# Optimization experiments

Hardware: AMD Instinct MI355X
Metric: run time of the kernel (lower is better)

Reference implementation:

```python
import jax, jax.numpy as jnp
import numpy as np

T, B = 32, 64
H, W = 16, 16
FEAT = 32
CNN_DIM = 512
N_ACT = 5
MAP_OUT = FEAT * H * W  # 8192, flattened map readout


def _conv_relu(x, w, b, stride):
    y = jax.lax.conv_general_dilated(
        x, w, (stride, stride), 'VALID',
        dimension_numbers=('NCHW', 'OIHW', 'NCHW'))
    return jax.nn.relu(y + b[None, :, None, None])


def _mlp(x, w1, b1, w2, b2):
    return jax.nn.relu(x @ w1 + b1) @ w2 + b2


def setup_inputs() -> dict:
    key = jax.random.key(0)
    ks = jax.random.split(key, 32)
    g = lambda k, shape, fan: jax.random.normal(k, shape, jnp.float32) * (1.0 / np.sqrt(fan))
    inp = {}
    inp['image'] = jax.random.uniform(ks[0], (T * B, 84, 84, 3), jnp.float32) * 255.0
    inp['done'] = jnp.zeros((T, B), jnp.float32)
    inp['state0'] = jnp.zeros((B, FEAT, H, W), jnp.float32)
    inp['position'] = jax.random.randint(ks[1], (T * B, 2), 0, H).astype(jnp.int32)
    # NatureCNN params
    inp['w1'] = g(ks[2], (32, 3, 8, 8), 3 * 8 * 8); inp['b1'] = jnp.zeros((32,), jnp.float32)
    inp['w2'] = g(ks[3], (64, 32, 4, 4), 32 * 4 * 4); inp['b2'] = jnp.zeros((64,), jnp.float32)
    inp['w3'] = g(ks[4], (64, 64, 3, 3), 64 * 3 * 3); inp['b3'] = jnp.zeros((64,), jnp.float32)
    inp['wfc'] = g(ks[5], (64 * 7 * 7, CNN_DIM), 64 * 7 * 7); inp['bfc'] = jnp.zeros((CNN_DIM,), jnp.float32)
    # Map write projection
    inp['Ww'] = g(ks[6], (CNN_DIM, FEAT), CNN_DIM); inp['bw'] = jnp.zeros((FEAT,), jnp.float32)
    # pos_net MLP: one-hot(16)+one-hot(16)=32 -> 64
    inp['wp1'] = g(ks[7], (2 * H, 64), 2 * H); inp['bp1'] = jnp.zeros((64,), jnp.float32)
    inp['wp2'] = g(ks[8], (64, 64), 64); inp['bp2'] = jnp.zeros((64,), jnp.float32)
    # policy MLP: (MAP_OUT+64) -> 64 -> N_ACT
    inp['wpo1'] = g(ks[9], (MAP_OUT + 64, 64), MAP_OUT + 64); inp['bpo1'] = jnp.zeros((64,), jnp.float32)
    inp['wpo2'] = g(ks[10], (64, N_ACT), 64) * 0.01; inp['bpo2'] = jnp.zeros((N_ACT,), jnp.float32)
    # value MLP
    inp['wv1'] = g(ks[11], (MAP_OUT + 64, 64), MAP_OUT + 64); inp['bv1'] = jnp.zeros((64,), jnp.float32)
    inp['wv2'] = g(ks[12], (64, 1), 64); inp['bv2'] = jnp.zeros((1,), jnp.float32)
    return inp


def reference(image, done, state0, w1, b1, w2, b2, w3, b3, wfc, bfc, Ww, bw,
              wp1, bp1, wp2, bp2, wpo1, bpo1, wpo2, bpo2, wv1, bv1, wv2, bv2,
              position):
    # preprocess_image: /255 and NHWC -> NCHW
    x = jnp.transpose(image / 255.0, (0, 3, 1, 2))
    x = _conv_relu(x, w1, b1, 4)   # [TB,32,20,20]
    x = _conv_relu(x, w2, b2, 2)   # [TB,64,9,9]
    x = _conv_relu(x, w3, b3, 1)   # [TB,64,7,7]
    h = jax.nn.relu(x.reshape(x.shape[0], -1) @ wfc + bfc)  # [TB,512]

    h_seq = h.reshape(T, B, CNN_DIM)
    idx_seq = position.reshape(T, B, 2)
    benv = jnp.arange(B)

    def step(state, inp):
        h_t, d_t, i_t = inp
        masked = (1.0 - d_t)[:, None, None, None] * state  # reset done envs
        wfeat = h_t @ Ww + bw                              # [B,FEAT]
        state = masked.at[benv, :, i_t[:, 0], i_t[:, 1]].add(wfeat)
        return state, state.reshape(B, -1)                 # per-step map readout

    state, outs = jax.lax.scan(step, state0, (h_seq, done, idx_seq))
    hidden = outs.reshape(T * B, MAP_OUT)

    # position net on one-hot coords
    pos_oh = jnp.concatenate([jax.nn.one_hot(position[:, 0], H, dtype=hidden.dtype),
                              jax.nn.one_hot(position[:, 1], W, dtype=hidden.dtype)], axis=1)
    pos_feat = _mlp(pos_oh, wp1, bp1, wp2, bp2)            # [TB,64]
    hidden = jnp.concatenate([hidden, pos_feat], axis=1)

    logits = _mlp(hidden, wpo1, bpo1, wpo2, bpo2)          # [TB,N_ACT]
    v = _mlp(hidden, wv1, bv1, wv2, bv2)                   # [TB,1]
    return logits, v, state
```

## Files before the change

kernel.cpp:

```cpp
#include <hip/hip_runtime.h>
#include <hip/hip_bf16.h>


#define TT 32
#define BB 64
#define TBR 2048

typedef _Float16 half_t;
typedef __attribute__((ext_vector_type(4))) _Float16 half4;
typedef __attribute__((ext_vector_type(8))) _Float16 half8;
typedef __attribute__((ext_vector_type(4))) float f32x4;

#define OFF_W1T   0u
#define OFF_W2T   6144u
#define OFF_W3T   22528u
#define OFF_WF    40960u
#define OFF_PF    106496u
#define OFF_Y0    237568u
#define OFF_YS    245760u
#define OFF_H     507904u
#define OFF_DELTA 1556480u
#define OFF_WFCT  1818624u
#define OFF_C3    2621440u
#define OFF_C2    5832704u
#define OFF_C1    11141120u

__global__ __launch_bounds__(256) void prep_all(
    const float* __restrict__ w1, const float* __restrict__ w2,
    const float* __restrict__ w3, half_t* __restrict__ w1p,
    half_t* __restrict__ w2T, half_t* __restrict__ w3T,
    const float* __restrict__ wfc, half_t* __restrict__ wfcT) {
  __shared__ float t[32][33];
  int bx = blockIdx.x;
  if (bx < 304) {
    int g = bx * 256 + threadIdx.x;
    if (g < 8192) {
      int kk = g & 31, oc = (g >> 5) & 31, tap = g >> 10;
      half_t v = (half_t)0.f;
      if (kk < 24) {
        int kx = kk / 3, c = kk - 3 * kx;
        v = (half_t)(w1[oc * 192 + c * 64 + tap * 8 + kx] * (1.0f / 255.0f));
      }
      w1p[g] = v;
      return;
    }
    int g2 = g - 8192;
    if (g2 < 32768) {
      int c = g2 & 31, oc = (g2 >> 5) & 63, tap = g2 >> 11;
      w2T[g2] = (half_t)w2[oc * 512 + c * 16 + tap];
      return;
    }
    int g3 = g2 - 32768;
    if (g3 < 36864) {
      int c = g3 & 63, oc = (g3 >> 6) & 63, tap = g3 >> 12;
      w3T[g3] = (half_t)w3[oc * 576 + c * 9 + tap];
    }
    return;
  }
  int gb = bx - 304;
  int k0 = (gb % 98) * 32, n0 = (gb / 98) * 32;
  int tx = threadIdx.x & 31, ty = threadIdx.x >> 5;
#pragma unroll
  for (int i = 0; i < 4; ++i)
    t[ty + 8 * i][tx] = wfc[(size_t)(k0 + ty + 8 * i) * 512 + n0 + tx];
  __syncthreads();
#pragma unroll
  for (int i = 0; i < 4; ++i)
    wfcT[(size_t)(n0 + ty + 8 * i) * 3136 + k0 + tx] =
        (half_t)t[tx][ty + 8 * i];
}

#define C1_BANDF 5040
#define C1_BANDV 1260
__global__ __launch_bounds__(256) void conv1_mfma(
    const float* __restrict__ img, const half_t* __restrict__ w1p,
    const float* __restrict__ b1, half_t* __restrict__ out, int n0) {
  __shared__ __align__(16) half_t As[2][C1_BANDF];
  int tid = threadIdx.x;
  int li = blockIdx.x;
  int w = tid >> 6, l = tid & 63, lc = l & 15, q = l >> 4;
  const float* ib = img + (size_t)(n0 + li) * 21168;
  half_t* ob = out + (size_t)li * 400 * 32;

  half8 bfrag[8][2];
#pragma unroll
  for (int tap = 0; tap < 8; ++tap)
#pragma unroll
    for (int t = 0; t < 2; ++t)
      bfrag[tap][t] =
          *(const half8*)(w1p + (size_t)(tap * 32 + t * 16 + lc) * 32 + q * 8);
  float b1v[2] = {b1[lc], b1[16 + lc]};

  f32x4 fr[5];
#define C1_LOADB(b)                                                   \
  {                                                                   \
    const float* src = ib + 4032 * (b);                               \
    _Pragma("unroll") for (int i = 0; i < 5; ++i) {                   \
      int g = tid + 256 * i;                                          \
      if (g < C1_BANDV) fr[i] = *(const f32x4*)(src + 4 * g);         \
    }                                                                 \
  }
#define C1_WRITEB(buf)                                                \
  {                                                                   \
    _Pragma("unroll") for (int i = 0; i < 5; ++i) {                   \
      int g = tid + 256 * i;                                          \
      if (g < C1_BANDV) {                                             \
        half4 o;                                                      \
        _Pragma("unroll") for (int j = 0; j < 4; ++j)                 \
            o[j] = (half_t)fr[i][j];                                  \
        *(half4*)&As[buf][4 * g] = o;                                 \
      }                                                               \
    }                                                                 \
  }

  C1_LOADB(0);
  C1_WRITEB(0);
  for (int b = 0; b < 5; ++b) {
    if (b < 4) C1_LOADB(b + 1);
    __syncthreads();
    int buf = b & 1;
    for (int tile = w; tile < 5; tile += 4) {
      int lp = tile * 16 + lc;
      int oyl = lp / 20, ox = lp - oyl * 20;
      f32x4 acc[2];
      acc[0] = (f32x4){0.f, 0.f, 0.f, 0.f};
      acc[1] = (f32x4){0.f, 0.f, 0.f, 0.f};
#pragma unroll
      for (int ky = 0; ky < 8; ++ky) {
        half8 af;
        if (q < 3) {
          const half_t* p = &As[buf][(4 * oyl + ky) * 252 + 12 * ox + q * 8];
          *(half4*)&af = *(const half4*)p;
          *((half4*)&af + 1) = *((const half4*)(p + 4));
        } else {
#pragma unroll
          for (int j = 0; j < 8; ++j) af[j] = (half_t)0.f;
        }
        acc[0] = __builtin_amdgcn_mfma_f32_16x16x32_f16(af, bfrag[ky][0],
                                                        acc[0], 0, 0, 0);
        acc[1] = __builtin_amdgcn_mfma_f32_16x16x32_f16(af, bfrag[ky][1],
                                                        acc[1], 0, 0, 0);
      }
#pragma unroll
      for (int t = 0; t < 2; ++t) {
#pragma unroll
        for (int r = 0; r < 4; ++r) {
          int mr = b * 80 + tile * 16 + q * 4 + r;
          ob[(size_t)mr * 32 + t * 16 + lc] =
              (half_t)fmaxf(acc[t][r] + b1v[t], 0.f);
        }
      }
    }
    if (b < 4) C1_WRITEB((b + 1) & 1);
  }
}

__global__ __launch_bounds__(256) void conv2_mfma(
    const half_t* __restrict__ in, const half_t* __restrict__ w2T,
    const float* __restrict__ b2, half_t* __restrict__ out, int n0) {
  __shared__ __align__(16) half_t As[12800];
  int tid = threadIdx.x;
  int li = blockIdx.x;
  int w = tid >> 6, l = tid & 63, lc = l & 15, q = l >> 4;
  const half_t* inb = in + (size_t)li * 12800;

#pragma unroll
  for (int i = 0; i < 7; ++i) {
    int ci = tid + 256 * i;
    if (ci < 1600) {
      uint4 v = *(const uint4*)(inb + ci * 8);
      int ip = ci >> 2, sp = ip >> 1;
      int u = ((ip & 1) << 6) | ((ci & 3) << 4);
      int byte = sp * 128 + (u ^ ((sp & 7) << 4));
      *(uint4*)((char*)As + byte) = v;
    }
  }

  half8 bfrag[16][2];
#pragma unroll
  for (int tap = 0; tap < 16; ++tap)
#pragma unroll
    for (int j = 0; j < 2; ++j) {
      int nt = (w & 1) * 2 + j;
      bfrag[tap][j] =
          *(const half8*)(w2T + (size_t)(tap * 64 + nt * 16 + lc) * 32 + q * 8);
    }
  float b2v[2];
#pragma unroll
  for (int j = 0; j < 2; ++j) b2v[j] = b2[(w & 1) * 32 + j * 16 + lc];

  __syncthreads();

  half_t* ob = out + (size_t)(n0 + li) * 5184;
#pragma unroll
  for (int ti = 0; ti < 3; ++ti) {
    int tile = (w >> 1) + 2 * ti;
    int row16 = tile * 16 + lc;
    int orow = row16 < 81 ? row16 : 80;
    int oy = orow / 9, ox = orow - oy * 9;
    f32x4 acc[2];
    acc[0] = (f32x4){0.f, 0.f, 0.f, 0.f};
    acc[1] = (f32x4){0.f, 0.f, 0.f, 0.f};
#pragma unroll
    for (int tap = 0; tap < 16; ++tap) {
      int ky = tap >> 2, kx = tap & 3;
      int ip = (2 * oy + ky) * 20 + 2 * ox + kx;
      int sp = ip >> 1;
      int u = ((ip & 1) << 6) | (q << 4);
      int byte = sp * 128 + (u ^ ((sp & 7) << 4));
      half8 af = *(const half8*)((const char*)As + byte);
      acc[0] = __builtin_amdgcn_mfma_f32_16x16x32_f16(af, bfrag[tap][0],
                                                      acc[0], 0, 0, 0);
      acc[1] = __builtin_amdgcn_mfma_f32_16x16x32_f16(af, bfrag[tap][1],
                                                      acc[1], 0, 0, 0);
    }
#pragma unroll
    for (int j = 0; j < 2; ++j) {
#pragma unroll
      for (int r = 0; r < 4; ++r) {
        int mr = tile * 16 + q * 4 + r;
        if (mr < 81) {
          int col = (w & 1) * 32 + j * 16 + lc;
          ob[(size_t)mr * 64 + col] = (half_t)fmaxf(acc[j][r] + b2v[j], 0.f);
        }
      }
    }
  }
}

__global__ __launch_bounds__(256) void conv3_mfma(
    const half_t* __restrict__ in, const half_t* __restrict__ w3T,
    const float* __restrict__ b3, half_t* __restrict__ out) {
  __shared__ __align__(16) half_t As[5184];
  int tid = threadIdx.x;
  int li = blockIdx.x;
  int w = tid >> 6, l = tid & 63, lc = l & 15, q = l >> 4;
  const half_t* inb = in + (size_t)li * 5184;

#pragma unroll
  for (int i = 0; i < 3; ++i) {
    int ci = tid + 256 * i;
    if (ci < 648) {
      uint4 v = *(const uint4*)(inb + ci * 8);
      int ir = ci >> 3, cc = ci & 7;
      int byte = ir * 128 + (((cc << 4)) ^ ((ir & 7) << 4));
      *(uint4*)((char*)As + byte) = v;
    }
  }

  half8 bfrag[9][2];
#pragma unroll
  for (int tap = 0; tap < 9; ++tap)
#pragma unroll
    for (int ch = 0; ch < 2; ++ch)
      bfrag[tap][ch] = *(const half8*)(
          w3T + (size_t)(tap * 64 + w * 16 + lc) * 64 + ch * 32 + q * 8);
  float b3v = b3[w * 16 + lc];

  __syncthreads();

  half_t* ob = out + (size_t)li * 3136;
#pragma unroll
  for (int tile = 0; tile < 4; ++tile) {
    int row16 = tile * 16 + lc;
    int orow = row16 < 49 ? row16 : 48;
    int oy = orow / 7, ox = orow - oy * 7;
    f32x4 acc = (f32x4){0.f, 0.f, 0.f, 0.f};
#pragma unroll
    for (int tap = 0; tap < 9; ++tap) {
      int ky = tap / 3, kx = tap - ky * 3;
      int ir = (oy + ky) * 9 + ox + kx;
#pragma unroll
      for (int ch = 0; ch < 2; ++ch) {
        int byte = ir * 128 + (((ch << 6) | (q << 4)) ^ ((ir & 7) << 4));
        half8 af = *(const half8*)((const char*)As + byte);
        acc = __builtin_amdgcn_mfma_f32_16x16x32_f16(af, bfrag[tap][ch],
                                                     acc, 0, 0, 0);
      }
    }
#pragma unroll
    for (int r = 0; r < 4; ++r) {
      int pos = tile * 16 + q * 4 + r;
      if (pos < 49) {
        int col = w * 16 + lc;
        ob[(size_t)col * 49 + pos] = (half_t)fmaxf(acc[r] + b3v, 0.f);
      }
    }
  }
}

__global__ __launch_bounds__(256) void fc_mfma(
    const half_t* __restrict__ A, const half_t* __restrict__ Bt,
    const float* __restrict__ bias, float* __restrict__ C) {
  __shared__ __align__(16) half_t As[64 * 40];
  __shared__ __align__(16) half_t Bs[64 * 40];
  int tid = threadIdx.x;
  int m0 = blockIdx.y * 64, n0 = blockIdx.x * 64;
  int w = tid >> 6;
  int l = tid & 63;
  int lc = l & 15, q = l >> 4;
  int srow = tid >> 2, sseg = tid & 3;

  const half_t* aPtr = A + (size_t)(m0 + srow) * 3136 + sseg * 8;
  const half_t* bPtr = Bt + (size_t)(n0 + srow) * 3136 + sseg * 8;
  uint4 aReg = *(const uint4*)aPtr;
  uint4 bReg = *(const uint4*)bPtr;

  f32x4 acc[4];
#pragma unroll
  for (int t = 0; t < 4; ++t) acc[t] = (f32x4){0.f, 0.f, 0.f, 0.f};

  for (int k0 = 0; k0 < 3136; k0 += 32) {
    __syncthreads();
    *(uint4*)&As[srow * 40 + sseg * 8] = aReg;
    *(uint4*)&Bs[srow * 40 + sseg * 8] = bReg;
    __syncthreads();
    if (k0 + 32 < 3136) {
      aReg = *(const uint4*)(aPtr + k0 + 32);
      bReg = *(const uint4*)(bPtr + k0 + 32);
    }
    half8 af = *(const half8*)&As[(w * 16 + lc) * 40 + q * 8];
#pragma unroll
    for (int t = 0; t < 4; ++t) {
      half8 bf = *(const half8*)&Bs[(t * 16 + lc) * 40 + q * 8];
      acc[t] = __builtin_amdgcn_mfma_f32_16x16x32_f16(af, bf, acc[t], 0, 0, 0);
    }
  }
#pragma unroll
  for (int t = 0; t < 4; ++t) {
#pragma unroll
    for (int r = 0; r < 4; ++r) {
      int row = m0 + w * 16 + q * 4 + r;
      int col = n0 + t * 16 + lc;
      C[(size_t)row * 512 + col] = fmaxf(acc[t][r] + bias[col], 0.f);
    }
  }
}

__global__ __launch_bounds__(256) void mid1_kernel(
    const float* __restrict__ h, const float* __restrict__ Ww,
    const float* __restrict__ bw, float* __restrict__ wf,
    const int* __restrict__ pos, const float* __restrict__ wp1,
    const float* __restrict__ bp1, const float* __restrict__ wp2,
    const float* __restrict__ bp2, float* __restrict__ pf,
    const float* __restrict__ s0, const float* __restrict__ wpo1,
    const float* __restrict__ wv1, float* __restrict__ y0) {
  __shared__ float red[128];
  int bx = blockIdx.x;
  if (bx < 256) {
    int g = bx * 256 + threadIdx.x;
    int row = g >> 5, oc = g & 31;
    float acc = bw[oc];
    const float* hr = h + (size_t)row * 512;
#pragma unroll 8
    for (int k = 0; k < 512; ++k) acc += hr[k] * Ww[k * 32 + oc];
    wf[g] = acc;
    return;
  }
  if (bx < 768) {
    int row = ((bx - 256) * 256 + threadIdx.x) >> 6;
    int l = threadIdx.x & 63;
    int p0 = pos[row * 2], p1 = pos[row * 2 + 1];
    float t1 = fmaxf(wp1[p0 * 64 + l] + wp1[(16 + p1) * 64 + l] + bp1[l], 0.f);
    float acc = bp2[l];
#pragma unroll
    for (int k = 0; k < 64; ++k) acc += __shfl(t1, k) * wp2[k * 64 + l];
    pf[row * 64 + l] = acc;
    return;
  }
  int g = bx - 768;
  int b = g >> 5, kc = g & 31;
  int n = threadIdx.x & 127, kh = threadIdx.x >> 7;
  const float* W = (n < 64) ? (wpo1 + n) : (wv1 + (n - 64));
  int k0 = kc * 256 + kh * 128;
  const float* s = s0 + (size_t)b * 8192 + k0;
  float acc = 0.f;
#pragma unroll 8
  for (int j = 0; j < 128; ++j) acc += s[j] * W[(size_t)(k0 + j) * 64];
  if (kh) red[n] = acc;
  __syncthreads();
  if (!kh) atomicAdd(y0 + b * 128 + n, acc + red[n]);
}

__global__ __launch_bounds__(256) void mid2_kernel(
    const int* __restrict__ pos, const float* __restrict__ wf,
    const float* __restrict__ wpo1, const float* __restrict__ wv1,
    float* __restrict__ delta, const float* __restrict__ s0,
    const float* __restrict__ done, float* __restrict__ out_state) {
  int bx = blockIdx.x;
  if (bx < 1024) {
    int row = bx * 2 + (threadIdx.x >> 7);
    int n = threadIdx.x & 127;
    const float* W = (n < 64) ? (wpo1 + n) : (wv1 + (n - 64));
    int off = pos[row * 2] * 16 + pos[row * 2 + 1];
    const float* wfr = wf + row * 32;
    float d = 0.f;
#pragma unroll
    for (int c = 0; c < 32; ++c) d += wfr[c] * W[(size_t)(c * 256 + off) * 64];
    delta[(size_t)row * 128 + n] = d;
    return;
  }
  int b = bx - 1024, tid = threadIdx.x;
  float s[32];
#pragma unroll
  for (int c = 0; c < 32; ++c) s[c] = s0[(size_t)b * 8192 + c * 256 + tid];
  for (int t = 0; t < TT; ++t) {
    int row = t * BB + b;
    float mask = 1.f - done[row];
    int off = pos[row * 2] * 16 + pos[row * 2 + 1];
#pragma unroll
    for (int c = 0; c < 32; ++c) s[c] *= mask;
    if (tid == off) {
#pragma unroll
      for (int c = 0; c < 32; ++c) s[c] += wf[row * 32 + c];
    }
  }
#pragma unroll
  for (int c = 0; c < 32; ++c) out_state[(size_t)b * 8192 + c * 256 + tid] = s[c];
}

__global__ __launch_bounds__(128) void scan_kernel(
    const float* __restrict__ y0, const float* __restrict__ done,
    const float* __restrict__ delta, float* __restrict__ ys) {
  int b = blockIdx.x;
  int n = threadIdx.x;
  float y = y0[b * 128 + n];
  for (int t = 0; t < TT; ++t) {
    int row = t * BB + b;
    y = y * (1.f - done[row]) + delta[(size_t)row * 128 + n];
    ys[(size_t)row * 128 + n] = y;
  }
}

__global__ __launch_bounds__(256) void head_kernel(
    const float* __restrict__ ys, const float* __restrict__ pf,
    const float* __restrict__ wpo1, const float* __restrict__ wv1,
    const float* __restrict__ bpo1, const float* __restrict__ bv1,
    const float* __restrict__ wpo2, const float* __restrict__ bpo2,
    const float* __restrict__ wv2, const float* __restrict__ bv2,
    float* __restrict__ logits, float* __restrict__ vout) {
  int row = (blockIdx.x * 256 + threadIdx.x) >> 6;
  int l = threadIdx.x & 63;
  float pfv = pf[row * 64 + l];
  float accp = bpo1[l] + ys[(size_t)row * 128 + l];
  float accv = bv1[l] + ys[(size_t)row * 128 + 64 + l];
#pragma unroll
  for (int k = 0; k < 64; ++k) {
    float pk = __shfl(pfv, k);
    accp += pk * wpo1[(size_t)(8192 + k) * 64 + l];
    accv += pk * wv1[(size_t)(8192 + k) * 64 + l];
  }
  float rp = fmaxf(accp, 0.f), rv = fmaxf(accv, 0.f);
#pragma unroll
  for (int a = 0; a < 5; ++a) {
    float pa = rp * wpo2[l * 5 + a];
#pragma unroll
    for (int m = 32; m >= 1; m >>= 1) pa += __shfl_xor(pa, m);
    if (l == 0) logits[row * 5 + a] = pa + bpo2[a];
  }
  float pv = rv * wv2[l];
#pragma unroll
  for (int m = 32; m >= 1; m >>= 1) pv += __shfl_xor(pv, m);
  if (l == 0) vout[row] = pv + bv2[0];
}

extern "C" void kernel_launch(void* const* d_in, const int* in_sizes, int n_in,
                              void* d_out, int out_size, void* d_ws, size_t ws_size,
                              hipStream_t stream) {
  const float* image = (const float*)d_in[0];
  const float* done = (const float*)d_in[1];
  const float* state0 = (const float*)d_in[2];
  const int* position = (const int*)d_in[3];
  const float* w1 = (const float*)d_in[4];
  const float* b1 = (const float*)d_in[5];
  const float* w2 = (const float*)d_in[6];
  const float* b2 = (const float*)d_in[7];
  const float* w3 = (const float*)d_in[8];
  const float* b3 = (const float*)d_in[9];
  const float* wfc = (const float*)d_in[10];
  const float* bfc = (const float*)d_in[11];
  const float* Ww = (const float*)d_in[12];
  const float* bw = (const float*)d_in[13];
  const float* wp1 = (const float*)d_in[14];
  const float* bp1 = (const float*)d_in[15];
  const float* wp2 = (const float*)d_in[16];
  const float* bp2 = (const float*)d_in[17];
  const float* wpo1 = (const float*)d_in[18];
  const float* bpo1 = (const float*)d_in[19];
  const float* wpo2 = (const float*)d_in[20];
  const float* bpo2 = (const float*)d_in[21];
  const float* wv1 = (const float*)d_in[22];
  const float* bv1 = (const float*)d_in[23];
  const float* wv2 = (const float*)d_in[24];
  const float* bv2 = (const float*)d_in[25];

  float* ws = (float*)d_ws;
  half_t* w1p = (half_t*)(ws + OFF_W1T);
  half_t* w2T = (half_t*)(ws + OFF_W2T);
  half_t* w3T = (half_t*)(ws + OFF_W3T);
  float* wf = ws + OFF_WF;
  float* pfb = ws + OFF_PF;
  float* y0 = ws + OFF_Y0;
  float* ysb = ws + OFF_YS;
  float* h = ws + OFF_H;
  float* deltab = ws + OFF_DELTA;
  half_t* wfcT = (half_t*)(ws + OFF_WFCT);
  half_t* c3b = (half_t*)(ws + OFF_C3);
  half_t* c2b = (half_t*)(ws + OFF_C2);
  half_t* c1b = (half_t*)(ws + OFF_C1);

  float* out = (float*)d_out;
  float* out_logits = out;
  float* out_v = out + 10240;
  float* out_state = out + 12288;

  int CS;
  if (ws_size >= (size_t)24248320 * 4) CS = 2048;
  else if (ws_size >= (size_t)17694720 * 4) CS = 1024;
  else CS = 512;
  int nc = TBR / CS;

  hipMemsetAsync(y0, 0, 8192 * sizeof(float), stream);
  prep_all<<<1872, 256, 0, stream>>>(w1, w2, w3, w1p, w2T, w3T, wfc, wfcT);

  for (int c = 0; c < nc; ++c) {
    int n0 = c * CS;
    conv1_mfma<<<CS, 256, 0, stream>>>(image, w1p, b1, c1b, n0);
    conv2_mfma<<<CS, 256, 0, stream>>>(c1b, w2T, b2, c2b, n0);
  }
  conv3_mfma<<<TBR, 256, 0, stream>>>(c2b, w3T, b3, c3b);
  fc_mfma<<<dim3(8, 32), 256, 0, stream>>>(c3b, wfcT, bfc, h);
  mid1_kernel<<<2816, 256, 0, stream>>>(h, Ww, bw, wf, position, wp1, bp1,
                                        wp2, bp2, pfb, state0, wpo1, wv1, y0);
  mid2_kernel<<<1088, 256, 0, stream>>>(position, wf, wpo1, wv1, deltab,
                                        state0, done, out_state);
  scan_kernel<<<64, 128, 0, stream>>>(y0, done, deltab, ysb);
  head_kernel<<<512, 256, 0, stream>>>(ysb, pfb, wpo1, wv1, bpo1, bv1,
                                       wpo2, bpo2, wv2, bv2, out_logits, out_v);
}
```

Baseline: 452.8 us.

## Split FC GEMM along K into two partial sums and double-buffer LDS

The FC GEMM now runs a split-K grid with two halves of the 3136-long reduction. Each half writes raw partial sums to its own buffer, and the second buffer reuses the conv2 scratch area. The bias add and ReLU move into mid1, which sums the two partials as it reads them. The shared-memory tiles are double-buffered, so each K step needs one barrier instead of two. This doubles the block count from 256 to 512 to fill more CUs, at the cost of extra fp32 partial-sum traffic and a combine step in mid1.

```diff
diff --git a/kernel.cpp b/kernel.cpp
--- a/kernel.cpp
+++ b/kernel.cpp
@@ -291,18 +291,19 @@
 
 __global__ __launch_bounds__(256) void fc_mfma(
     const half_t* __restrict__ A, const half_t* __restrict__ Bt,
-    const float* __restrict__ bias, float* __restrict__ C) {
-  __shared__ __align__(16) half_t As[64 * 40];
-  __shared__ __align__(16) half_t Bs[64 * 40];
+    float* __restrict__ h0, float* __restrict__ h1) {
+  __shared__ __align__(16) half_t As[2][64 * 40];
+  __shared__ __align__(16) half_t Bs[2][64 * 40];
   int tid = threadIdx.x;
   int m0 = blockIdx.y * 64, n0 = blockIdx.x * 64;
+  int kh = blockIdx.z;
   int w = tid >> 6;
   int l = tid & 63;
   int lc = l & 15, q = l >> 4;
   int srow = tid >> 2, sseg = tid & 3;
 
-  const half_t* aPtr = A + (size_t)(m0 + srow) * 3136 + sseg * 8;
-  const half_t* bPtr = Bt + (size_t)(n0 + srow) * 3136 + sseg * 8;
+  const half_t* aPtr = A + (size_t)(m0 + srow) * 3136 + kh * 1568 + sseg * 8;
+  const half_t* bPtr = Bt + (size_t)(n0 + srow) * 3136 + kh * 1568 + sseg * 8;
   uint4 aReg = *(const uint4*)aPtr;
   uint4 bReg = *(const uint4*)bPtr;
 
@@ -310,35 +311,37 @@
 #pragma unroll
   for (int t = 0; t < 4; ++t) acc[t] = (f32x4){0.f, 0.f, 0.f, 0.f};
 
-  for (int k0 = 0; k0 < 3136; k0 += 32) {
+  for (int s = 0; s < 49; ++s) {
+    int cur = s & 1;
+    *(uint4*)&As[cur][srow * 40 + sseg * 8] = aReg;
+    *(uint4*)&Bs[cur][srow * 40 + sseg * 8] = bReg;
     __syncthreads();
-    *(uint4*)&As[srow * 40 + sseg * 8] = aReg;
-    *(uint4*)&Bs[srow * 40 + sseg * 8] = bReg;
-    __syncthreads();
-    if (k0 + 32 < 3136) {
-      aReg = *(const uint4*)(aPtr + k0 + 32);
-      bReg = *(const uint4*)(bPtr + k0 + 32);
-    }
-    half8 af = *(const half8*)&As[(w * 16 + lc) * 40 + q * 8];
+    if (s < 48) {
+      aReg = *(const uint4*)(aPtr + (s + 1) * 32);
+      bReg = *(const uint4*)(bPtr + (s + 1) * 32);
+    }
+    half8 af = *(const half8*)&As[cur][(w * 16 + lc) * 40 + q * 8];
 #pragma unroll
     for (int t = 0; t < 4; ++t) {
-      half8 bf = *(const half8*)&Bs[(t * 16 + lc) * 40 + q * 8];
+      half8 bf = *(const half8*)&Bs[cur][(t * 16 + lc) * 40 + q * 8];
       acc[t] = __builtin_amdgcn_mfma_f32_16x16x32_f16(af, bf, acc[t], 0, 0, 0);
     }
   }
+  float* H = kh ? h1 : h0;
 #pragma unroll
   for (int t = 0; t < 4; ++t) {
 #pragma unroll
     for (int r = 0; r < 4; ++r) {
       int row = m0 + w * 16 + q * 4 + r;
       int col = n0 + t * 16 + lc;
-      C[(size_t)row * 512 + col] = fmaxf(acc[t][r] + bias[col], 0.f);
+      H[(size_t)row * 512 + col] = acc[t][r];
     }
   }
 }
 
 __global__ __launch_bounds__(256) void mid1_kernel(
-    const float* __restrict__ h, const float* __restrict__ Ww,
+    const float* __restrict__ h0, const float* __restrict__ h1,
+    const float* __restrict__ bfc, const float* __restrict__ Ww,
     const float* __restrict__ bw, float* __restrict__ wf,
     const int* __restrict__ pos, const float* __restrict__ wp1,
     const float* __restrict__ bp1, const float* __restrict__ wp2,
@@ -351,9 +354,11 @@
     int g = bx * 256 + threadIdx.x;
     int row = g >> 5, oc = g & 31;
     float acc = bw[oc];
-    const float* hr = h + (size_t)row * 512;
+    const float* hr0 = h0 + (size_t)row * 512;
+    const float* hr1 = h1 + (size_t)row * 512;
 #pragma unroll 8
-    for (int k = 0; k < 512; ++k) acc += hr[k] * Ww[k * 32 + oc];
+    for (int k = 0; k < 512; ++k)
+      acc += fmaxf(hr0[k] + hr1[k] + bfc[k], 0.f) * Ww[k * 32 + oc];
     wf[g] = acc;
     return;
   }
@@ -502,7 +507,8 @@
   float* pfb = ws + OFF_PF;
   float* y0 = ws + OFF_Y0;
   float* ysb = ws + OFF_YS;
-  float* h = ws + OFF_H;
+  float* h0b = ws + OFF_H;
+  float* h1b = ws + OFF_C2;
   float* deltab = ws + OFF_DELTA;
   half_t* wfcT = (half_t*)(ws + OFF_WFCT);
   half_t* c3b = (half_t*)(ws + OFF_C3);
@@ -529,9 +535,10 @@
     conv2_mfma<<<CS, 256, 0, stream>>>(c1b, w2T, b2, c2b, n0);
   }
   conv3_mfma<<<TBR, 256, 0, stream>>>(c2b, w3T, b3, c3b);
-  fc_mfma<<<dim3(8, 32), 256, 0, stream>>>(c3b, wfcT, bfc, h);
-  mid1_kernel<<<2816, 256, 0, stream>>>(h, Ww, bw, wf, position, wp1, bp1,
-                                        wp2, bp2, pfb, state0, wpo1, wv1, y0);
+  fc_mfma<<<dim3(8, 32, 2), 256, 0, stream>>>(c3b, wfcT, h0b, h1b);
+  mid1_kernel<<<2816, 256, 0, stream>>>(h0b, h1b, bfc, Ww, bw, wf, position,
+                                        wp1, bp1, wp2, bp2, pfb, state0,
+                                        wpo1, wv1, y0);
   mid2_kernel<<<1088, 256, 0, stream>>>(position, wf, wpo1, wv1, deltab,
                                         state0, done, out_state);
   scan_kernel<<<64, 128, 0, stream>>>(y0, done, deltab, ysb);
```

New measurement: 450.3 us. Within noise of the previous version (-0.6%).
